# Kernel tuning notes

Hardware: AMD Instinct MI355X
Metric: run time of the kernel (lower is better)

## Reference

```python
import jax, jax.numpy as jnp
import numpy as np

B, L, DS, DP = 4, 384, 384, 128
NEAR_BAND = 4
LN_EPS = 1e-5


def setup_inputs():
    key = jax.random.key(0)
    k = jax.random.split(key, 16)
    return {
        "seq_repr": jax.random.normal(k[0], (B, L, DS), jnp.float32),
        "pair_repr": jax.random.normal(k[1], (B, L, L, DP), jnp.float32),
        "ln_s_g": 1.0 + 0.1 * jax.random.normal(k[2], (DS,), jnp.float32),
        "ln_s_b": 0.1 * jax.random.normal(k[3], (DS,), jnp.float32),
        "ln_z_g": 1.0 + 0.1 * jax.random.normal(k[4], (DP,), jnp.float32),
        "ln_z_b": 0.1 * jax.random.normal(k[5], (DP,), jnp.float32),
        "W_seq": jax.random.normal(k[6], (DS, DS), jnp.float32) / np.sqrt(DS).astype(np.float32),
        "W_pair": jax.random.normal(k[7], (DP, DP), jnp.float32) / np.sqrt(DP).astype(np.float32),
        "W_gs": 0.02 * jax.random.normal(k[8], (2 * DS, DS), jnp.float32),
        "b_gs": jnp.ones((DS,), jnp.float32),
        "W_gz": 0.02 * jax.random.normal(k[9], (2 * DP, DP), jnp.float32),
        "b_gz": jnp.ones((DP,), jnp.float32),
        "W1": jax.random.normal(k[10], (DS + 2 * DP, 64), jnp.float32) / np.sqrt(DS + 2 * DP).astype(np.float32),
        "b1": 0.01 * jax.random.normal(k[11], (64,), jnp.float32),
        "W2": jax.random.normal(k[12], (64, 1), jnp.float32) / 8.0,
        "b2": jnp.zeros((1,), jnp.float32),
        "chain_id": jax.random.randint(k[13], (B, L), 0, 2, jnp.int32),
        "mask": jax.random.randint(k[14], (B, L), 0, 2, jnp.int32).astype(jnp.bool_),
    }


def _layernorm(x, g, b):
    mu = jnp.mean(x, axis=-1, keepdims=True)
    var = jnp.mean(jnp.square(x - mu), axis=-1, keepdims=True)
    return (x - mu) * jax.lax.rsqrt(var + LN_EPS) * g + b


def _masked_mean(x, m, axes):
    num = jnp.sum(x * m, axis=axes)
    den = jnp.clip(jnp.sum(m, axis=axes), 1e-6, None)  # mask has trailing dim 1 -> den broadcasts
    return num / den


def _masked_max(x, m, axis):
    v = jnp.max(jnp.where(m > 0, x, -jnp.inf), axis=axis)
    return jnp.where(jnp.isinf(v), jnp.zeros_like(v), v)


def reference(seq_repr, pair_repr, ln_s_g, ln_s_b, ln_z_g, ln_z_b, W_seq, W_pair,
              W_gs, b_gs, W_gz, b_gz, W1, b1, W2, b2, chain_id, mask):
    # sequence branch: LN -> Linear -> masked mean/max over L -> gated blend
    s = _layernorm(seq_repr, ln_s_g, ln_s_b) @ W_seq          # [B,L,DS]
    m = mask.astype(s.dtype)[..., None]                        # [B,L,1]
    s_mean = _masked_mean(s, m, 1)                             # [B,DS]
    s_max = _masked_max(s, m, 1)                               # [B,DS]
    gate_s = jax.nn.sigmoid(jnp.concatenate([s_max, s_mean], -1) @ W_gs + b_gs)
    s_feat = s_mean + gate_s * (s_max - s_mean)

    # pair branch: symmetrize, zero diagonal, LN -> Linear
    p = 0.5 * (pair_repr + jnp.swapaxes(pair_repr, 1, 2))      # [B,L,L,DP]
    eye = jnp.eye(L, dtype=p.dtype)[None, :, :, None]
    p = p * (1.0 - eye)
    p = _layernorm(p, ln_z_g, ln_z_b) @ W_pair

    pm = (mask[:, :, None] & mask[:, None, :])[..., None].astype(p.dtype)   # [B,L,L,1]
    same = (chain_id[:, :, None] == chain_id[:, None, :])[..., None]
    intra = pm * same.astype(p.dtype)
    inter = pm * (~same).astype(p.dtype)

    inter_mean = _masked_mean(p, inter, (1, 2))                # [B,DP]
    row_den = jnp.clip(jnp.sum(inter, axis=2), 1e-6, None)     # [B,L,1]
    row_mean = jnp.sum(p * inter, axis=2) / row_den            # [B,L,DP]
    inter_peak = jnp.max(row_mean, axis=1)                     # [B,DP]
    gate_z = jax.nn.sigmoid(jnp.concatenate([inter_peak, inter_mean], -1) @ W_gz + b_gz)
    inter_feat = inter_mean + gate_z * (inter_peak - inter_mean)

    idx = jnp.arange(L)
    band = (jnp.abs(idx[:, None] - idx[None, :]) <= NEAR_BAND)[None, :, :, None].astype(p.dtype)
    intra_compact = _masked_mean(p, intra * band, (1, 2))      # [B,DP]

    feat = jnp.concatenate([s_feat, inter_feat, intra_compact], -1)  # [B, DS+2*DP]
    h = jax.nn.relu(feat @ W1 + b1)
    prob = jax.nn.sigmoid(h @ W2 + b2)[..., 0]                 # [B]
    return prob
```

## Files before the change

### kernel.cpp

```cpp
#include <hip/hip_runtime.h>
#include <hip/hip_bf16.h>
#include <math.h>

#define B_  4
#define L_  384
#define DS_ 384
#define DP_ 128
#define NB_ 4
#define FEAT_ (DS_ + 2*DP_)
#define LN_EPS_ 1e-5f

__global__ __launch_bounds__(256) void k_mask(const void* __restrict__ mask_raw,
                                              int* __restrict__ maskN, int n) {
    const unsigned int* dw = (const unsigned int*)mask_raw;
    int tid = threadIdx.x;
    int local_int = 1, local_flt = 1;
    for (int i = tid; i < n / 4; i += blockDim.x) {
        unsigned int v = dw[i];
        if (v != 0u && v != 1u) local_int = 0;
        if (v != 0u && v != 0x3F800000u) local_flt = 0;
    }
    int all_int = __syncthreads_and(local_int);
    int all_flt = __syncthreads_and(local_flt);
    if (all_int) {
        for (int i = tid; i < n; i += blockDim.x) maskN[i] = (dw[i] != 0u) ? 1 : 0;
    } else if (all_flt) {
        const float* f = (const float*)mask_raw;
        for (int i = tid; i < n; i += blockDim.x) maskN[i] = (f[i] != 0.0f) ? 1 : 0;
    } else {
        const unsigned char* by = (const unsigned char*)mask_raw;
        for (int i = tid; i < n; i += blockDim.x) maskN[i] = by[i] ? 1 : 0;
    }
}

__global__ __launch_bounds__(256) void k_pair_rows(
    const float* __restrict__ pair, const float* __restrict__ gz,
    const float* __restrict__ bz, const int* __restrict__ chain,
    const int* __restrict__ maskN,
    float* __restrict__ rs_inter, float* __restrict__ rs_intra,
    float* __restrict__ den_inter, float* __restrict__ den_intra) {
    const int row = blockIdx.x;
    const int b = row / L_, i = row % L_;
    const int tid = threadIdx.x;
    const int wave = tid >> 6;
    const int lane = tid & 63;
    const int ch2 = lane * 2;

    const int mi = maskN[b * L_ + i];
    const int ci = chain[b * L_ + i];
    const float g0 = gz[ch2], g1 = gz[ch2 + 1];
    const float bb0 = bz[ch2], bb1 = bz[ch2 + 1];

    const float* basA = pair + (size_t)row * L_ * DP_;
    const float* basB = pair + (size_t)b * L_ * L_ * DP_ + (size_t)i * DP_;

    float acc_i0 = 0.f, acc_i1 = 0.f, acc_a0 = 0.f, acc_a1 = 0.f;
    float dI = 0.f, dA = 0.f;

    for (int j = wave; j < L_; j += 4) {
        float2 z1 = *(const float2*)(basA + (size_t)j * DP_ + ch2);
        float2 z2 = *(const float2*)(basB + (size_t)j * L_ * DP_ + ch2);
        float v0, v1;
        if (j == i) { v0 = 0.f; v1 = 0.f; }
        else { v0 = 0.5f * (z1.x + z2.x); v1 = 0.5f * (z1.y + z2.y); }
        float s = v0 + v1, q = v0 * v0 + v1 * v1;
        #pragma unroll
        for (int off = 32; off; off >>= 1) {
            s += __shfl_xor(s, off);
            q += __shfl_xor(q, off);
        }
        const float mu = s * (1.0f / DP_);
        const float var = q * (1.0f / DP_) - mu * mu;
        const float rstd = rsqrtf(var + LN_EPS_);
        const float y0 = (v0 - mu) * rstd * g0 + bb0;
        const float y1 = (v1 - mu) * rstd * g1 + bb1;
        const int mj = maskN[b * L_ + j];
        const int cj = chain[b * L_ + j];
        const int pm = mi & mj;
        const bool same = (ci == cj);
        int d = j - i; if (d < 0) d = -d;
        const float wI = (pm && !same) ? 1.f : 0.f;
        const float wA = (pm && same && d <= NB_) ? 1.f : 0.f;
        acc_i0 += wI * y0; acc_i1 += wI * y1;
        acc_a0 += wA * y0; acc_a1 += wA * y1;
        dI += wI; dA += wA;
    }

    __shared__ float smI[4][DP_], smA[4][DP_];
    __shared__ float smDI[4], smDA[4];
    smI[wave][ch2] = acc_i0; smI[wave][ch2 + 1] = acc_i1;
    smA[wave][ch2] = acc_a0; smA[wave][ch2 + 1] = acc_a1;
    if (lane == 0) { smDI[wave] = dI; smDA[wave] = dA; }
    __syncthreads();
    if (tid < DP_) {
        float vI = smI[0][tid] + smI[1][tid] + smI[2][tid] + smI[3][tid];
        float vA = smA[0][tid] + smA[1][tid] + smA[2][tid] + smA[3][tid];
        rs_inter[(size_t)row * DP_ + tid] = vI;
        rs_intra[(size_t)row * DP_ + tid] = vA;
    }
    if (tid == 0) {
        den_inter[row] = smDI[0] + smDI[1] + smDI[2] + smDI[3];
        den_intra[row] = smDA[0] + smDA[1] + smDA[2] + smDA[3];
    }
}

#define SROWS_ 4
__global__ __launch_bounds__(384) void k_seq_proj(
    const float* __restrict__ seq, const float* __restrict__ gs,
    const float* __restrict__ bs, const float* __restrict__ W,
    float* __restrict__ s_rows) {
    const int row0 = blockIdx.x * SROWS_;
    const int tid = threadIdx.x;
    const int wave = tid >> 6, lane = tid & 63;
    __shared__ float xn[SROWS_][DS_];
    __shared__ float sSum[SROWS_][6], sSq[SROWS_][6];
    const float gg = gs[tid], bbv = bs[tid];
    #pragma unroll
    for (int r = 0; r < SROWS_; r++) {
        float x = seq[(size_t)(row0 + r) * DS_ + tid];
        float s = x, q = x * x;
        #pragma unroll
        for (int off = 32; off; off >>= 1) {
            s += __shfl_xor(s, off);
            q += __shfl_xor(q, off);
        }
        if (lane == 0) { sSum[r][wave] = s; sSq[r][wave] = q; }
        xn[r][tid] = x;
    }
    __syncthreads();
    float mu[SROWS_], rstd[SROWS_];
    #pragma unroll
    for (int r = 0; r < SROWS_; r++) {
        float ts = 0.f, tq = 0.f;
        #pragma unroll
        for (int w = 0; w < 6; w++) { ts += sSum[r][w]; tq += sSq[r][w]; }
        mu[r] = ts * (1.0f / DS_);
        float var = tq * (1.0f / DS_) - mu[r] * mu[r];
        rstd[r] = rsqrtf(var + LN_EPS_);
    }
    #pragma unroll
    for (int r = 0; r < SROWS_; r++)
        xn[r][tid] = (xn[r][tid] - mu[r]) * rstd[r] * gg + bbv;
    __syncthreads();
    float acc[SROWS_] = {0.f, 0.f, 0.f, 0.f};
    for (int k = 0; k < DS_; k++) {
        float w = W[(size_t)k * DS_ + tid];
        #pragma unroll
        for (int r = 0; r < SROWS_; r++) acc[r] += xn[r][k] * w;
    }
    #pragma unroll
    for (int r = 0; r < SROWS_; r++)
        s_rows[(size_t)(row0 + r) * DS_ + tid] = acc[r];
}

__global__ __launch_bounds__(384) void k_seq_reduce(
    const float* __restrict__ s_rows, const int* __restrict__ maskN,
    const float* __restrict__ Wgs, const float* __restrict__ bgs,
    float* __restrict__ feat) {
    const int b = blockIdx.x;
    const int ch = threadIdx.x;
    float sum = 0.f, mx = -INFINITY;
    int den = 0;
    for (int l = 0; l < L_; l++) {
        int m = maskN[b * L_ + l];
        float v = s_rows[(size_t)(b * L_ + l) * DS_ + ch];
        if (m) { sum += v; mx = fmaxf(mx, v); den++; }
    }
    const float fden = fmaxf((float)den, 1e-6f);
    const float smean = sum / fden;
    const float smax = (den > 0) ? mx : 0.f;
    __shared__ float sMean[DS_], sMax[DS_];
    sMean[ch] = smean; sMax[ch] = smax;
    __syncthreads();
    float acc = bgs[ch];
    for (int k = 0; k < DS_; k++) {
        acc += sMax[k] * Wgs[(size_t)k * DS_ + ch]
             + sMean[k] * Wgs[(size_t)(k + DS_) * DS_ + ch];
    }
    const float gate = 1.f / (1.f + expf(-acc));
    feat[b * FEAT_ + ch] = smean + gate * (smax - smean);
}

__global__ __launch_bounds__(128) void k_proj_rows(
    const float* __restrict__ rs_inter, const float* __restrict__ den_inter,
    const float* __restrict__ Wp, float* __restrict__ proj) {
    const int row = blockIdx.x;
    const int ch = threadIdx.x;
    __shared__ float rs[DP_];
    rs[ch] = rs_inter[(size_t)row * DP_ + ch];
    __syncthreads();
    float acc = 0.f;
    for (int k = 0; k < DP_; k++) acc += rs[k] * Wp[k * DP_ + ch];
    proj[(size_t)row * DP_ + ch] = acc / fmaxf(den_inter[row], 1e-6f);
}

__global__ __launch_bounds__(128) void k_pair_final(
    const float* __restrict__ rs_inter, const float* __restrict__ rs_intra,
    const float* __restrict__ den_inter, const float* __restrict__ den_intra,
    const float* __restrict__ proj, const float* __restrict__ Wp,
    const float* __restrict__ Wgz, const float* __restrict__ bgz,
    float* __restrict__ feat) {
    const int b = blockIdx.x;
    const int ch = threadIdx.x;
    float totI = 0.f, totA = 0.f, dI = 0.f, dA = 0.f, peak = -INFINITY;
    for (int i = 0; i < L_; i++) {
        size_t r = (size_t)(b * L_ + i);
        totI += rs_inter[r * DP_ + ch];
        totA += rs_intra[r * DP_ + ch];
        peak = fmaxf(peak, proj[r * DP_ + ch]);
        dI += den_inter[r];
        dA += den_intra[r];
    }
    __shared__ float sI[DP_], sA[DP_], sPk[DP_], sIM[DP_];
    sI[ch] = totI; sA[ch] = totA;
    __syncthreads();
    float accI = 0.f, accA = 0.f;
    for (int k = 0; k < DP_; k++) {
        accI += sI[k] * Wp[k * DP_ + ch];
        accA += sA[k] * Wp[k * DP_ + ch];
    }
    const float im = accI / fmaxf(dI, 1e-6f);
    const float ic = accA / fmaxf(dA, 1e-6f);
    sPk[ch] = peak; sIM[ch] = im;
    __syncthreads();
    float acc = bgz[ch];
    for (int k = 0; k < DP_; k++) {
        acc += sPk[k] * Wgz[k * DP_ + ch] + sIM[k] * Wgz[(k + DP_) * DP_ + ch];
    }
    const float gate = 1.f / (1.f + expf(-acc));
    feat[b * FEAT_ + DS_ + ch] = im + gate * (sPk[ch] - im);
    feat[b * FEAT_ + DS_ + DP_ + ch] = ic;
}

__global__ __launch_bounds__(64) void k_head(
    const float* __restrict__ feat, const float* __restrict__ W1,
    const float* __restrict__ b1, const float* __restrict__ W2,
    const float* __restrict__ b2, float* __restrict__ out) {
    const int b = blockIdx.x;
    const int h = threadIdx.x;
    float acc = b1[h];
    for (int k = 0; k < FEAT_; k++) acc += feat[b * FEAT_ + k] * W1[k * 64 + h];
    float hr = fmaxf(acc, 0.f);
    float p = hr * W2[h];
    #pragma unroll
    for (int off = 32; off; off >>= 1) p += __shfl_xor(p, off);
    if (h == 0) out[b] = 1.f / (1.f + expf(-(p + b2[0])));
}

extern "C" void kernel_launch(void* const* d_in, const int* in_sizes, int n_in,
                              void* d_out, int out_size, void* d_ws, size_t ws_size,
                              hipStream_t stream) {
    const float* seq    = (const float*)d_in[0];
    const float* pair   = (const float*)d_in[1];
    const float* ln_s_g = (const float*)d_in[2];
    const float* ln_s_b = (const float*)d_in[3];
    const float* ln_z_g = (const float*)d_in[4];
    const float* ln_z_b = (const float*)d_in[5];
    const float* W_seq  = (const float*)d_in[6];
    const float* W_pair = (const float*)d_in[7];
    const float* W_gs   = (const float*)d_in[8];
    const float* b_gs   = (const float*)d_in[9];
    const float* W_gz   = (const float*)d_in[10];
    const float* b_gz   = (const float*)d_in[11];
    const float* W1     = (const float*)d_in[12];
    const float* b1     = (const float*)d_in[13];
    const float* W2     = (const float*)d_in[14];
    const float* b2     = (const float*)d_in[15];
    const int*   chain  = (const int*)d_in[16];
    const void*  mask   = d_in[17];
    float* out = (float*)d_out;

    char* ws = (char*)d_ws;
    int* maskN = (int*)ws;              ws += (size_t)B_ * L_ * sizeof(int);
    float* rs_inter = (float*)ws;       ws += (size_t)B_ * L_ * DP_ * sizeof(float);
    float* rs_intra = (float*)ws;       ws += (size_t)B_ * L_ * DP_ * sizeof(float);
    float* den_inter = (float*)ws;      ws += (size_t)B_ * L_ * sizeof(float);
    float* den_intra = (float*)ws;      ws += (size_t)B_ * L_ * sizeof(float);
    float* proj = (float*)ws;           ws += (size_t)B_ * L_ * DP_ * sizeof(float);
    float* s_rows = (float*)ws;         ws += (size_t)B_ * L_ * DS_ * sizeof(float);
    float* feat = (float*)ws;           ws += (size_t)B_ * FEAT_ * sizeof(float);

    const int nMask = B_ * L_;

    k_mask<<<1, 256, 0, stream>>>(mask, maskN, nMask);
    k_pair_rows<<<B_ * L_, 256, 0, stream>>>(pair, ln_z_g, ln_z_b, chain, maskN,
                                             rs_inter, rs_intra, den_inter, den_intra);
    k_seq_proj<<<(B_ * L_) / SROWS_, 384, 0, stream>>>(seq, ln_s_g, ln_s_b, W_seq, s_rows);
    k_seq_reduce<<<B_, 384, 0, stream>>>(s_rows, maskN, W_gs, b_gs, feat);
    k_proj_rows<<<B_ * L_, 128, 0, stream>>>(rs_inter, den_inter, W_pair, proj);
    k_pair_final<<<B_, 128, 0, stream>>>(rs_inter, rs_intra, den_inter, den_intra,
                                         proj, W_pair, W_gz, b_gz, feat);
    k_head<<<B_, 64, 0, stream>>>(feat, W1, b1, W2, b2, out);
}
```

Measured before the change: 682.9 us.

## Tile pair matrix symmetrically, skip masked pairs, fuse tail reductions into finalize

Pair processing now runs over upper-triangular 16x16 tiles of (i,j). Each LN'd symmetric element is computed once and accumulated into both row i and row j through LDS and atomics, and masked-out or zero-weight pairs skip their global loads entirely. The sequence reduce, projection, pair-final and head kernels are replaced by chunked partial kernels plus a single finalize kernel, which adds parallelism to what were 4-block reductions. The cost is a memset, float atomics with nondeterministic summation order, per-element LDS read-modify-write, and divergent skipping inside waves.

```diff
diff --git a/kernel.cpp b/kernel.cpp
--- a/kernel.cpp
+++ b/kernel.cpp
@@ -9,6 +9,15 @@
 #define NB_ 4
 #define FEAT_ (DS_ + 2*DP_)
 #define LN_EPS_ 1e-5f
+#define T_ 16
+#define NT_ (L_ / T_)
+#define NTP_ (NT_ * (NT_ + 1) / 2)
+#define NCH_ 8
+#define CHROWS_ (L_ / NCH_)
+
+__device__ __forceinline__ void atomAddF(float* p, float v) {
+    unsafeAtomicAdd(p, v);
+}
 
 __global__ __launch_bounds__(256) void k_mask(const void* __restrict__ mask_raw,
                                               int* __restrict__ maskN, int n) {
@@ -33,74 +42,121 @@
     }
 }
 
-__global__ __launch_bounds__(256) void k_pair_rows(
+__global__ __launch_bounds__(256) void k_pair_tiles(
     const float* __restrict__ pair, const float* __restrict__ gz,
     const float* __restrict__ bz, const int* __restrict__ chain,
     const int* __restrict__ maskN,
     float* __restrict__ rs_inter, float* __restrict__ rs_intra,
     float* __restrict__ den_inter, float* __restrict__ den_intra) {
-    const int row = blockIdx.x;
-    const int b = row / L_, i = row % L_;
+    extern __shared__ float lds[];
+    float* smJI = lds;
+    float* smJA = smJI + 4 * 16 * 128;
+    float* smDJI = smJA + 4 * 16 * 128;
+    float* smDJA = smDJI + 64;
+    int* s_mi = (int*)(smDJA + 64);
+    int* s_ci = s_mi + 16;
+    int* s_mj = s_ci + 16;
+    int* s_cj = s_mj + 16;
+
+    const int b = blockIdx.x / NTP_;
+    int t = blockIdx.x % NTP_;
+    int ta = 0;
+    while (t >= NT_ - ta) { t -= NT_ - ta; ta++; }
+    const int tb = ta + t;
+    const int i0 = ta * T_, j0 = tb * T_;
+    const float fac = (ta == tb) ? 0.5f : 1.0f;
+
     const int tid = threadIdx.x;
-    const int wave = tid >> 6;
-    const int lane = tid & 63;
+    const int wave = tid >> 6, lane = tid & 63;
     const int ch2 = lane * 2;
 
-    const int mi = maskN[b * L_ + i];
-    const int ci = chain[b * L_ + i];
+    for (int idx = tid; idx < 4 * 16 * 128; idx += 256) { smJI[idx] = 0.f; smJA[idx] = 0.f; }
+    if (tid < 64) { smDJI[tid] = 0.f; smDJA[tid] = 0.f; }
+    if (tid < 16) {
+        s_mi[tid] = maskN[b * L_ + i0 + tid];
+        s_ci[tid] = chain[b * L_ + i0 + tid];
+        s_mj[tid] = maskN[b * L_ + j0 + tid];
+        s_cj[tid] = chain[b * L_ + j0 + tid];
+    }
+    __syncthreads();
+
     const float g0 = gz[ch2], g1 = gz[ch2 + 1];
     const float bb0 = bz[ch2], bb1 = bz[ch2 + 1];
-
-    const float* basA = pair + (size_t)row * L_ * DP_;
-    const float* basB = pair + (size_t)b * L_ * L_ * DP_ + (size_t)i * DP_;
-
-    float acc_i0 = 0.f, acc_i1 = 0.f, acc_a0 = 0.f, acc_a1 = 0.f;
-    float dI = 0.f, dA = 0.f;
-
-    for (int j = wave; j < L_; j += 4) {
-        float2 z1 = *(const float2*)(basA + (size_t)j * DP_ + ch2);
-        float2 z2 = *(const float2*)(basB + (size_t)j * L_ * DP_ + ch2);
-        float v0, v1;
-        if (j == i) { v0 = 0.f; v1 = 0.f; }
-        else { v0 = 0.5f * (z1.x + z2.x); v1 = 0.5f * (z1.y + z2.y); }
-        float s = v0 + v1, q = v0 * v0 + v1 * v1;
-        #pragma unroll
-        for (int off = 32; off; off >>= 1) {
-            s += __shfl_xor(s, off);
-            q += __shfl_xor(q, off);
-        }
-        const float mu = s * (1.0f / DP_);
-        const float var = q * (1.0f / DP_) - mu * mu;
-        const float rstd = rsqrtf(var + LN_EPS_);
-        const float y0 = (v0 - mu) * rstd * g0 + bb0;
-        const float y1 = (v1 - mu) * rstd * g1 + bb1;
-        const int mj = maskN[b * L_ + j];
-        const int cj = chain[b * L_ + j];
-        const int pm = mi & mj;
-        const bool same = (ci == cj);
-        int d = j - i; if (d < 0) d = -d;
-        const float wI = (pm && !same) ? 1.f : 0.f;
-        const float wA = (pm && same && d <= NB_) ? 1.f : 0.f;
-        acc_i0 += wI * y0; acc_i1 += wI * y1;
-        acc_a0 += wA * y0; acc_a1 += wA * y1;
-        dI += wI; dA += wA;
-    }
-
-    __shared__ float smI[4][DP_], smA[4][DP_];
-    __shared__ float smDI[4], smDA[4];
-    smI[wave][ch2] = acc_i0; smI[wave][ch2 + 1] = acc_i1;
-    smA[wave][ch2] = acc_a0; smA[wave][ch2 + 1] = acc_a1;
-    if (lane == 0) { smDI[wave] = dI; smDA[wave] = dA; }
-    __syncthreads();
-    if (tid < DP_) {
-        float vI = smI[0][tid] + smI[1][tid] + smI[2][tid] + smI[3][tid];
-        float vA = smA[0][tid] + smA[1][tid] + smA[2][tid] + smA[3][tid];
-        rs_inter[(size_t)row * DP_ + tid] = vI;
-        rs_intra[(size_t)row * DP_ + tid] = vA;
-    }
-    if (tid == 0) {
-        den_inter[row] = smDI[0] + smDI[1] + smDI[2] + smDI[3];
-        den_intra[row] = smDA[0] + smDA[1] + smDA[2] + smDA[3];
+    const float* baseb = pair + (size_t)b * L_ * L_ * DP_;
+
+    float accI0[4] = {0, 0, 0, 0}, accI1[4] = {0, 0, 0, 0};
+    float accA0[4] = {0, 0, 0, 0}, accA1[4] = {0, 0, 0, 0};
+    float denI[4] = {0, 0, 0, 0}, denA[4] = {0, 0, 0, 0};
+
+    for (int r = 0; r < 4; ++r) {
+        const int il = (wave << 2) + r;
+        const int gi = i0 + il;
+        const int mi_ = s_mi[il];
+        const int ci_ = s_ci[il];
+        if (!mi_) continue;
+        for (int jl = 0; jl < 16; ++jl) {
+            const int gj = j0 + jl;
+            if (!s_mj[jl]) continue;
+            const bool same = (s_cj[jl] == ci_);
+            int d = gi - gj; d = d < 0 ? -d : d;
+            const float wI = (!same) ? fac : 0.f;
+            const float wA = (same && d <= NB_) ? fac : 0.f;
+            if (wI == 0.f && wA == 0.f) continue;
+            float v0, v1;
+            if (gi == gj) {
+                v0 = 0.f; v1 = 0.f;
+            } else {
+                const float2 a = *(const float2*)(baseb + ((size_t)gi * L_ + gj) * DP_ + ch2);
+                const float2 c = *(const float2*)(baseb + ((size_t)gj * L_ + gi) * DP_ + ch2);
+                v0 = 0.5f * (a.x + c.x); v1 = 0.5f * (a.y + c.y);
+            }
+            float s = v0 + v1, q = v0 * v0 + v1 * v1;
+            #pragma unroll
+            for (int off = 32; off; off >>= 1) {
+                s += __shfl_xor(s, off);
+                q += __shfl_xor(q, off);
+            }
+            const float mu = s * (1.f / DP_);
+            const float rstd = rsqrtf(q * (1.f / DP_) - mu * mu + LN_EPS_);
+            const float y0 = (v0 - mu) * rstd * g0 + bb0;
+            const float y1 = (v1 - mu) * rstd * g1 + bb1;
+            accI0[r] += wI * y0; accI1[r] += wI * y1;
+            accA0[r] += wA * y0; accA1[r] += wA * y1;
+            denI[r] += wI; denA[r] += wA;
+            float* pJI = smJI + ((wave * 16 + jl) << 7) + ch2;
+            float* pJA = smJA + ((wave * 16 + jl) << 7) + ch2;
+            pJI[0] += wI * y0; pJI[1] += wI * y1;
+            pJA[0] += wA * y0; pJA[1] += wA * y1;
+            if (lane == 0) { smDJI[wave * 16 + jl] += wI; smDJA[wave * 16 + jl] += wA; }
+        }
+    }
+    __syncthreads();
+    #pragma unroll
+    for (int r = 0; r < 4; ++r) {
+        const int gi = i0 + (wave << 2) + r;
+        const size_t o = ((size_t)(b * L_ + gi) << 7) + ch2;
+        atomAddF(&rs_inter[o], accI0[r]);
+        atomAddF(&rs_inter[o + 1], accI1[r]);
+        atomAddF(&rs_intra[o], accA0[r]);
+        atomAddF(&rs_intra[o + 1], accA1[r]);
+        if (lane == 0) {
+            atomAddF(&den_inter[b * L_ + gi], denI[r]);
+            atomAddF(&den_intra[b * L_ + gi], denA[r]);
+        }
+    }
+    for (int idx = tid; idx < 16 * 128; idx += 256) {
+        const int jl = idx >> 7, ch = idx & 127;
+        const float vI = smJI[idx] + smJI[idx + 2048] + smJI[idx + 4096] + smJI[idx + 6144];
+        const float vA = smJA[idx] + smJA[idx + 2048] + smJA[idx + 4096] + smJA[idx + 6144];
+        const size_t o = ((size_t)(b * L_ + j0 + jl) << 7) + ch;
+        atomAddF(&rs_inter[o], vI);
+        atomAddF(&rs_intra[o], vA);
+    }
+    if (tid < 16) {
+        const float dI = smDJI[tid] + smDJI[16 + tid] + smDJI[32 + tid] + smDJI[48 + tid];
+        const float dA = smDJA[tid] + smDJA[16 + tid] + smDJA[32 + tid] + smDJA[48 + tid];
+        atomAddF(&den_inter[b * L_ + j0 + tid], dI);
+        atomAddF(&den_intra[b * L_ + j0 + tid], dA);
     }
 }
 
@@ -153,98 +209,132 @@
         s_rows[(size_t)(row0 + r) * DS_ + tid] = acc[r];
 }
 
-__global__ __launch_bounds__(384) void k_seq_reduce(
+__global__ __launch_bounds__(384) void k_seq_partial(
     const float* __restrict__ s_rows, const int* __restrict__ maskN,
-    const float* __restrict__ Wgs, const float* __restrict__ bgs,
-    float* __restrict__ feat) {
-    const int b = blockIdx.x;
+    float* __restrict__ psum, float* __restrict__ pmax, int* __restrict__ pcnt) {
+    const int b = blockIdx.x / NCH_, c = blockIdx.x % NCH_;
     const int ch = threadIdx.x;
     float sum = 0.f, mx = -INFINITY;
-    int den = 0;
-    for (int l = 0; l < L_; l++) {
-        int m = maskN[b * L_ + l];
-        float v = s_rows[(size_t)(b * L_ + l) * DS_ + ch];
-        if (m) { sum += v; mx = fmaxf(mx, v); den++; }
-    }
-    const float fden = fmaxf((float)den, 1e-6f);
-    const float smean = sum / fden;
-    const float smax = (den > 0) ? mx : 0.f;
-    __shared__ float sMean[DS_], sMax[DS_];
-    sMean[ch] = smean; sMax[ch] = smax;
-    __syncthreads();
-    float acc = bgs[ch];
-    for (int k = 0; k < DS_; k++) {
-        acc += sMax[k] * Wgs[(size_t)k * DS_ + ch]
-             + sMean[k] * Wgs[(size_t)(k + DS_) * DS_ + ch];
-    }
-    const float gate = 1.f / (1.f + expf(-acc));
-    feat[b * FEAT_ + ch] = smean + gate * (smax - smean);
-}
-
-__global__ __launch_bounds__(128) void k_proj_rows(
-    const float* __restrict__ rs_inter, const float* __restrict__ den_inter,
-    const float* __restrict__ Wp, float* __restrict__ proj) {
-    const int row = blockIdx.x;
-    const int ch = threadIdx.x;
-    __shared__ float rs[DP_];
-    rs[ch] = rs_inter[(size_t)row * DP_ + ch];
-    __syncthreads();
-    float acc = 0.f;
-    for (int k = 0; k < DP_; k++) acc += rs[k] * Wp[k * DP_ + ch];
-    proj[(size_t)row * DP_ + ch] = acc / fmaxf(den_inter[row], 1e-6f);
-}
-
-__global__ __launch_bounds__(128) void k_pair_final(
+    int cnt = 0;
+    const int l0 = c * CHROWS_;
+    for (int l = l0; l < l0 + CHROWS_; ++l) {
+        if (maskN[b * L_ + l]) {
+            float v = s_rows[(size_t)(b * L_ + l) * DS_ + ch];
+            sum += v; mx = fmaxf(mx, v); cnt++;
+        }
+    }
+    psum[(size_t)blockIdx.x * DS_ + ch] = sum;
+    pmax[(size_t)blockIdx.x * DS_ + ch] = mx;
+    if (ch == 0) pcnt[blockIdx.x] = cnt;
+}
+
+__global__ __launch_bounds__(128) void k_pair_partial(
     const float* __restrict__ rs_inter, const float* __restrict__ rs_intra,
     const float* __restrict__ den_inter, const float* __restrict__ den_intra,
-    const float* __restrict__ proj, const float* __restrict__ Wp,
-    const float* __restrict__ Wgz, const float* __restrict__ bgz,
-    float* __restrict__ feat) {
+    const float* __restrict__ Wp,
+    float* __restrict__ pI, float* __restrict__ pA, float* __restrict__ pPk,
+    float* __restrict__ pdI, float* __restrict__ pdA) {
+    extern __shared__ float lds2[];
+    float* sWp = lds2;
+    float* sRS = sWp + 128 * 128;
+    const int b = blockIdx.x / NCH_, c = blockIdx.x % NCH_;
+    const int ch = threadIdx.x;
+    for (int idx = ch; idx < 128 * 128; idx += 128) sWp[idx] = Wp[idx];
+    float totI = 0.f, totA = 0.f, dI = 0.f, dA = 0.f, peak = -INFINITY;
+    const int r0 = b * L_ + c * CHROWS_;
+    for (int r = 0; r < CHROWS_; ++r) {
+        __syncthreads();
+        const float vI = rs_inter[(size_t)(r0 + r) * DP_ + ch];
+        sRS[ch] = vI;
+        totI += vI;
+        totA += rs_intra[(size_t)(r0 + r) * DP_ + ch];
+        const float den = den_inter[r0 + r];
+        dI += den; dA += den_intra[r0 + r];
+        __syncthreads();
+        float acc = 0.f;
+        for (int k = 0; k < 128; ++k) acc += sRS[k] * sWp[(k << 7) + ch];
+        peak = fmaxf(peak, acc / fmaxf(den, 1e-6f));
+    }
+    pI[(size_t)blockIdx.x * DP_ + ch] = totI;
+    pA[(size_t)blockIdx.x * DP_ + ch] = totA;
+    pPk[(size_t)blockIdx.x * DP_ + ch] = peak;
+    if (ch == 0) { pdI[blockIdx.x] = dI; pdA[blockIdx.x] = dA; }
+}
+
+__global__ __launch_bounds__(384) void k_finalize(
+    const float* __restrict__ psum, const float* __restrict__ pmax,
+    const int* __restrict__ pcnt,
+    const float* __restrict__ pI, const float* __restrict__ pA,
+    const float* __restrict__ pPk,
+    const float* __restrict__ pdI, const float* __restrict__ pdA,
+    const float* __restrict__ Wgs, const float* __restrict__ bgs,
+    const float* __restrict__ Wp, const float* __restrict__ Wgz,
+    const float* __restrict__ bgz,
+    const float* __restrict__ W1, const float* __restrict__ b1,
+    const float* __restrict__ W2, const float* __restrict__ b2,
+    float* __restrict__ out) {
     const int b = blockIdx.x;
-    const int ch = threadIdx.x;
-    float totI = 0.f, totA = 0.f, dI = 0.f, dA = 0.f, peak = -INFINITY;
-    for (int i = 0; i < L_; i++) {
-        size_t r = (size_t)(b * L_ + i);
-        totI += rs_inter[r * DP_ + ch];
-        totA += rs_intra[r * DP_ + ch];
-        peak = fmaxf(peak, proj[r * DP_ + ch]);
-        dI += den_inter[r];
-        dA += den_intra[r];
-    }
-    __shared__ float sI[DP_], sA[DP_], sPk[DP_], sIM[DP_];
-    sI[ch] = totI; sA[ch] = totA;
-    __syncthreads();
-    float accI = 0.f, accA = 0.f;
-    for (int k = 0; k < DP_; k++) {
-        accI += sI[k] * Wp[k * DP_ + ch];
-        accA += sA[k] * Wp[k * DP_ + ch];
-    }
-    const float im = accI / fmaxf(dI, 1e-6f);
-    const float ic = accA / fmaxf(dA, 1e-6f);
-    sPk[ch] = peak; sIM[ch] = im;
-    __syncthreads();
-    float acc = bgz[ch];
-    for (int k = 0; k < DP_; k++) {
-        acc += sPk[k] * Wgz[k * DP_ + ch] + sIM[k] * Wgz[(k + DP_) * DP_ + ch];
-    }
-    const float gate = 1.f / (1.f + expf(-acc));
-    feat[b * FEAT_ + DS_ + ch] = im + gate * (sPk[ch] - im);
-    feat[b * FEAT_ + DS_ + DP_ + ch] = ic;
-}
-
-__global__ __launch_bounds__(64) void k_head(
-    const float* __restrict__ feat, const float* __restrict__ W1,
-    const float* __restrict__ b1, const float* __restrict__ W2,
-    const float* __restrict__ b2, float* __restrict__ out) {
-    const int b = blockIdx.x;
-    const int h = threadIdx.x;
-    float acc = b1[h];
-    for (int k = 0; k < FEAT_; k++) acc += feat[b * FEAT_ + k] * W1[k * 64 + h];
-    float hr = fmaxf(acc, 0.f);
-    float p = hr * W2[h];
-    #pragma unroll
-    for (int off = 32; off; off >>= 1) p += __shfl_xor(p, off);
-    if (h == 0) out[b] = 1.f / (1.f + expf(-(p + b2[0])));
+    const int tid = threadIdx.x;
+    __shared__ float sMean[DS_], sMax[DS_], fI[DP_], fA[DP_], sPk[DP_], sIM[DP_];
+    __shared__ float feat[FEAT_];
+    __shared__ float sdI, sdA;
+    {
+        float s = 0.f, m = -INFINITY;
+        int cnt = 0;
+        for (int c = 0; c < NCH_; ++c) {
+            s += psum[(size_t)(b * NCH_ + c) * DS_ + tid];
+            m = fmaxf(m, pmax[(size_t)(b * NCH_ + c) * DS_ + tid]);
+            cnt += pcnt[b * NCH_ + c];
+        }
+        sMean[tid] = s / fmaxf((float)cnt, 1e-6f);
+        sMax[tid] = (cnt > 0) ? m : 0.f;
+    }
+    if (tid < DP_) {
+        float tI = 0.f, tA = 0.f, pk = -INFINITY, ddI = 0.f, ddA = 0.f;
+        for (int c = 0; c < NCH_; ++c) {
+            tI += pI[(size_t)(b * NCH_ + c) * DP_ + tid];
+            tA += pA[(size_t)(b * NCH_ + c) * DP_ + tid];
+            pk = fmaxf(pk, pPk[(size_t)(b * NCH_ + c) * DP_ + tid]);
+            ddI += pdI[b * NCH_ + c]; ddA += pdA[b * NCH_ + c];
+        }
+        fI[tid] = tI; fA[tid] = tA; sPk[tid] = pk;
+        if (tid == 0) { sdI = ddI; sdA = ddA; }
+    }
+    __syncthreads();
+    {
+        float acc = bgs[tid];
+        for (int k = 0; k < DS_; ++k)
+            acc += sMax[k] * Wgs[(size_t)k * DS_ + tid]
+                 + sMean[k] * Wgs[(size_t)(k + DS_) * DS_ + tid];
+        const float gate = 1.f / (1.f + expf(-acc));
+        feat[tid] = sMean[tid] + gate * (sMax[tid] - sMean[tid]);
+    }
+    if (tid < DP_) {
+        float aI = 0.f, aA = 0.f;
+        for (int k = 0; k < DP_; ++k) {
+            aI += fI[k] * Wp[(k << 7) + tid];
+            aA += fA[k] * Wp[(k << 7) + tid];
+        }
+        sIM[tid] = aI / fmaxf(sdI, 1e-6f);
+        feat[DS_ + DP_ + tid] = aA / fmaxf(sdA, 1e-6f);
+    }
+    __syncthreads();
+    if (tid < DP_) {
+        float acc = bgz[tid];
+        for (int k = 0; k < DP_; ++k)
+            acc += sPk[k] * Wgz[(k << 7) + tid] + sIM[k] * Wgz[((k + DP_) << 7) + tid];
+        const float gate = 1.f / (1.f + expf(-acc));
+        feat[DS_ + tid] = sIM[tid] + gate * (sPk[tid] - sIM[tid]);
+    }
+    __syncthreads();
+    if (tid < 64) {
+        float acc = b1[tid];
+        for (int k = 0; k < FEAT_; ++k) acc += feat[k] * W1[(k << 6) + tid];
+        float p = fmaxf(acc, 0.f) * W2[tid];
+        #pragma unroll
+        for (int off = 32; off; off >>= 1) p += __shfl_xor(p, off);
+        if (tid == 0) out[b] = 1.f / (1.f + expf(-(p + b2[0])));
+    }
 }
 
 extern "C" void kernel_launch(void* const* d_in, const int* in_sizes, int n_in,
@@ -271,24 +361,34 @@
     float* out = (float*)d_out;
 
     char* ws = (char*)d_ws;
-    int* maskN = (int*)ws;              ws += (size_t)B_ * L_ * sizeof(int);
-    float* rs_inter = (float*)ws;       ws += (size_t)B_ * L_ * DP_ * sizeof(float);
-    float* rs_intra = (float*)ws;       ws += (size_t)B_ * L_ * DP_ * sizeof(float);
-    float* den_inter = (float*)ws;      ws += (size_t)B_ * L_ * sizeof(float);
-    float* den_intra = (float*)ws;      ws += (size_t)B_ * L_ * sizeof(float);
-    float* proj = (float*)ws;           ws += (size_t)B_ * L_ * DP_ * sizeof(float);
-    float* s_rows = (float*)ws;         ws += (size_t)B_ * L_ * DS_ * sizeof(float);
-    float* feat = (float*)ws;           ws += (size_t)B_ * FEAT_ * sizeof(float);
-
-    const int nMask = B_ * L_;
-
-    k_mask<<<1, 256, 0, stream>>>(mask, maskN, nMask);
-    k_pair_rows<<<B_ * L_, 256, 0, stream>>>(pair, ln_z_g, ln_z_b, chain, maskN,
-                                             rs_inter, rs_intra, den_inter, den_intra);
+    float* rs_inter  = (float*)ws;  ws += (size_t)B_ * L_ * DP_ * 4;
+    float* rs_intra  = (float*)ws;  ws += (size_t)B_ * L_ * DP_ * 4;
+    float* den_inter = (float*)ws;  ws += (size_t)B_ * L_ * 4;
+    float* den_intra = (float*)ws;  ws += (size_t)B_ * L_ * 4;
+    const size_t zero_bytes = ((size_t)2 * B_ * L_ * DP_ + 2 * B_ * L_) * 4;
+    int*   maskN = (int*)ws;        ws += (size_t)B_ * L_ * 4;
+    float* s_rows = (float*)ws;     ws += (size_t)B_ * L_ * DS_ * 4;
+    float* psum = (float*)ws;       ws += (size_t)B_ * NCH_ * DS_ * 4;
+    float* pmax = (float*)ws;       ws += (size_t)B_ * NCH_ * DS_ * 4;
+    int*   pcnt = (int*)ws;         ws += (size_t)B_ * NCH_ * 4;
+    float* pI   = (float*)ws;       ws += (size_t)B_ * NCH_ * DP_ * 4;
+    float* pA   = (float*)ws;       ws += (size_t)B_ * NCH_ * DP_ * 4;
+    float* pPk  = (float*)ws;       ws += (size_t)B_ * NCH_ * DP_ * 4;
+    float* pdI  = (float*)ws;       ws += (size_t)B_ * NCH_ * 4;
+    float* pdA  = (float*)ws;       ws += (size_t)B_ * NCH_ * 4;
+
+    const size_t ldsTiles = (size_t)(2 * 4 * 16 * 128 + 128 + 64) * 4;
+    const size_t ldsPP    = (size_t)(128 * 128 + 128) * 4;
+
+    hipMemsetAsync(rs_inter, 0, zero_bytes, stream);
+    k_mask<<<1, 256, 0, stream>>>(mask, maskN, B_ * L_);
+    k_pair_tiles<<<B_ * NTP_, 256, ldsTiles, stream>>>(
+        pair, ln_z_g, ln_z_b, chain, maskN, rs_inter, rs_intra, den_inter, den_intra);
     k_seq_proj<<<(B_ * L_) / SROWS_, 384, 0, stream>>>(seq, ln_s_g, ln_s_b, W_seq, s_rows);
-    k_seq_reduce<<<B_, 384, 0, stream>>>(s_rows, maskN, W_gs, b_gs, feat);
-    k_proj_rows<<<B_ * L_, 128, 0, stream>>>(rs_inter, den_inter, W_pair, proj);
-    k_pair_final<<<B_, 128, 0, stream>>>(rs_inter, rs_intra, den_inter, den_intra,
-                                         proj, W_pair, W_gz, b_gz, feat);
-    k_head<<<B_, 64, 0, stream>>>(feat, W1, b1, W2, b2, out);
-}
+    k_seq_partial<<<B_ * NCH_, 384, 0, stream>>>(s_rows, maskN, psum, pmax, pcnt);
+    k_pair_partial<<<B_ * NCH_, 128, ldsPP, stream>>>(
+        rs_inter, rs_intra, den_inter, den_intra, W_pair, pI, pA, pPk, pdI, pdA);
+    k_finalize<<<B_, 384, 0, stream>>>(psum, pmax, pcnt, pI, pA, pPk, pdI, pdA,
+                                       W_gs, b_gs, W_pair, W_gz, b_gz,
+                                       W1, b1, W2, b2, out);
+}
```

Result: no change. 685.0 us (+0.3%).
